# Kernel tuning notes

Measured on AMD Instinct MI355X. Metric: run time of the kernel, lower is better.

The kernel has to match this reference:

```python
import jax, jax.numpy as jnp
import numpy as np

N_NODES = 100000
N_EDGES = 1000000
D_IN = 64
D_OUT = 64


def setup_inputs() -> dict:
    key = jax.random.key(0)
    k1, k2, k3, k4, k5 = jax.random.split(key, 5)
    x = jax.random.normal(k1, (N_NODES, D_IN), dtype=jnp.float32)
    edge_val = jax.random.uniform(k2, (N_EDGES,), dtype=jnp.float32)
    # 'he' initializer: randn(in, out) * sqrt(2/in)
    weight = jax.random.normal(k3, (D_IN, D_OUT), dtype=jnp.float32) * np.sqrt(2.0 / D_IN)
    edge_src = jax.random.randint(k4, (N_EDGES,), 0, N_NODES, dtype=jnp.int32)
    edge_dst = jax.random.randint(k5, (N_EDGES,), 0, N_NODES, dtype=jnp.int32)
    return {"x": x, "edge_val": edge_val, "weight": weight,
            "edge_src": edge_src, "edge_dst": edge_dst}


def reference(x, edge_val, weight, edge_src, edge_dst):
    # order == 'AW': out = A @ x (SpMM over edge list) then @ W
    msgs = edge_val[:, None] * x[edge_src]                      # [E, D_IN]
    agg = jax.ops.segment_sum(msgs, edge_dst, num_segments=N_NODES)  # [N, D_IN]
    out = agg @ weight                                          # [N, D_OUT]
    # embnormalize: F.normalize(out, p=2, dim=1) with eps=1e-12
    norm = jnp.linalg.norm(out, axis=1, keepdims=True)
    out = out / jnp.maximum(norm, 1e-12)
    return jax.nn.relu(out)
```

## Files before the change

kernel.cpp:

```cpp
#include <hip/hip_runtime.h>
#include <hip/hip_bf16.h>

#define D 64

__global__ __launch_bounds__(256) void hist_kernel(
    const int* __restrict__ edge_dst, int* __restrict__ counts, int nEdges)
{
    int i = blockIdx.x * blockDim.x + threadIdx.x;
    int stride = gridDim.x * blockDim.x;
    for (; i < nEdges; i += stride)
        atomicAdd(&counts[edge_dst[i]], 1);
}

__global__ __launch_bounds__(256) void scanA_kernel(
    const int* __restrict__ counts, int* __restrict__ incl,
    int* __restrict__ blockSums, int n)
{
    __shared__ int buf[256];
    const int i = blockIdx.x * 256 + threadIdx.x;
    int v = (i < n) ? counts[i] : 0;
    buf[threadIdx.x] = v;
    __syncthreads();
    for (int off = 1; off < 256; off <<= 1) {
        int t = (threadIdx.x >= off) ? buf[threadIdx.x - off] : 0;
        __syncthreads();
        buf[threadIdx.x] += t;
        __syncthreads();
    }
    if (i < n) incl[i] = buf[threadIdx.x];
    if (threadIdx.x == 255) blockSums[blockIdx.x] = buf[255];
}

__global__ __launch_bounds__(1024) void scanB_kernel(int* __restrict__ bs, int nB)
{
    __shared__ int buf[1024];
    __shared__ int carry;
    if (threadIdx.x == 0) carry = 0;
    __syncthreads();
    for (int base = 0; base < nB; base += 1024) {
        const int i = base + (int)threadIdx.x;
        int v = (i < nB) ? bs[i] : 0;
        buf[threadIdx.x] = v;
        __syncthreads();
        for (int off = 1; off < 1024; off <<= 1) {
            int t = (threadIdx.x >= off) ? buf[threadIdx.x - off] : 0;
            __syncthreads();
            buf[threadIdx.x] += t;
            __syncthreads();
        }
        if (i < nB) bs[i] = buf[threadIdx.x] - v + carry;
        __syncthreads();
        if (threadIdx.x == 0) carry += buf[1023];
        __syncthreads();
    }
}

__global__ __launch_bounds__(256) void scanC_kernel(
    const int* __restrict__ counts, const int* __restrict__ incl,
    const int* __restrict__ blockSums, int* __restrict__ offsets,
    int* __restrict__ cursor, int n)
{
    const int i = blockIdx.x * 256 + threadIdx.x;
    if (i < n) {
        int off = incl[i] - counts[i] + blockSums[blockIdx.x];
        offsets[i] = off;
        cursor[i]  = off;
    }
}

__global__ __launch_bounds__(256) void scatter_kernel(
    const int*   __restrict__ edge_src,
    const int*   __restrict__ edge_dst,
    const float* __restrict__ edge_val,
    int*  __restrict__ cursor,
    int2* __restrict__ sorted_sv,
    int nEdges)
{
    int i = blockIdx.x * blockDim.x + threadIdx.x;
    int stride = gridDim.x * blockDim.x;
    for (; i < nEdges; i += stride) {
        const int d = edge_dst[i];
        const int pos = atomicAdd(&cursor[d], 1);
        sorted_sv[pos] = make_int2(edge_src[i], __float_as_int(edge_val[i]));
    }
}

__global__ __launch_bounds__(256) void gather_gemv_norm_kernel(
    const float* __restrict__ x,
    const float* __restrict__ W,
    const int*   __restrict__ offsets,
    const int*   __restrict__ counts,
    const int2*  __restrict__ sorted_sv,
    float*       __restrict__ out,
    int nNodes)
{
    __shared__ float Wlds[D * D];
    for (int i = threadIdx.x; i < D * D; i += blockDim.x)
        Wlds[i] = W[i];
    __syncthreads();

    const int lane   = threadIdx.x & 63;
    const int wave   = (blockIdx.x * blockDim.x + threadIdx.x) >> 6;
    const int nWaves = (gridDim.x * blockDim.x) >> 6;

    for (int n = wave; n < nNodes; n += nWaves) {
        const int start = offsets[n];
        const int cnt   = counts[n];

        float a0 = 0.f, a1 = 0.f, a2 = 0.f, a3 = 0.f;
        int j = start;
        const int end4 = start + (cnt & ~3);
        for (; j < end4; j += 4) {
            const int2 e0 = sorted_sv[j + 0];
            const int2 e1 = sorted_sv[j + 1];
            const int2 e2 = sorted_sv[j + 2];
            const int2 e3 = sorted_sv[j + 3];
            a0 += __int_as_float(e0.y) * x[(size_t)e0.x * D + lane];
            a1 += __int_as_float(e1.y) * x[(size_t)e1.x * D + lane];
            a2 += __int_as_float(e2.y) * x[(size_t)e2.x * D + lane];
            a3 += __int_as_float(e3.y) * x[(size_t)e3.x * D + lane];
        }
        const int end = start + cnt;
        for (; j < end; ++j) {
            const int2 e = sorted_sv[j];
            a0 += __int_as_float(e.y) * x[(size_t)e.x * D + lane];
        }
        const float acc = (a0 + a1) + (a2 + a3);

        float o = 0.f;
        #pragma unroll
        for (int k = 0; k < D; ++k)
            o += __shfl(acc, k, 64) * Wlds[k * D + lane];

        float ss = o * o;
        #pragma unroll
        for (int off = 32; off; off >>= 1)
            ss += __shfl_xor(ss, off, 64);
        const float inv = 1.f / fmaxf(sqrtf(ss), 1e-12f);

        out[(size_t)n * D + lane] = fmaxf(o * inv, 0.f);
    }
}

extern "C" void kernel_launch(void* const* d_in, const int* in_sizes, int n_in,
                              void* d_out, int out_size, void* d_ws, size_t ws_size,
                              hipStream_t stream)
{
    const float* x        = (const float*)d_in[0];
    const float* edge_val = (const float*)d_in[1];
    const float* weight   = (const float*)d_in[2];
    const int*   edge_src = (const int*)d_in[3];
    const int*   edge_dst = (const int*)d_in[4];

    const int nNodes = in_sizes[0] / D;
    const int nEdges = in_sizes[1];
    const int nB     = (nNodes + 255) / 256;

    int*  counts    = (int*)d_ws;
    int*  offsets   = counts  + nNodes;
    int*  cursor    = offsets + nNodes;
    int*  incl      = cursor  + nNodes;
    int*  blockSums = incl    + nNodes;
    int2* sorted_sv = (int2*)(blockSums + 4096);
    float* out      = (float*)d_out;

    hipMemsetAsync(counts, 0, (size_t)nNodes * sizeof(int), stream);

    hist_kernel<<<2048, 256, 0, stream>>>(edge_dst, counts, nEdges);

    scanA_kernel<<<nB, 256, 0, stream>>>(counts, incl, blockSums, nNodes);
    scanB_kernel<<<1, 1024, 0, stream>>>(blockSums, nB);
    scanC_kernel<<<nB, 256, 0, stream>>>(counts, incl, blockSums, offsets, cursor, nNodes);

    scatter_kernel<<<2048, 256, 0, stream>>>(
        edge_src, edge_dst, edge_val, cursor, sorted_sv, nEdges);

    gather_gemv_norm_kernel<<<2048, 256, 0, stream>>>(
        x, weight, offsets, counts, sorted_sv, out, nNodes);
}
```

Baseline: 356.1 us.

## Gather fp16 copy of x, fuse conversion into histogram, drop scan pass

Converts x to half precision inside the histogram kernel and gathers the half rows in the aggregation kernel, halving gather traffic. The single-block scanB pass is removed: each scanC block sums the preceding block totals itself. The GEMV now reads a transposed, padded W and the accumulator from LDS with float4 loads instead of 64 shuffles, and the scatter grid is doubled. This adds fp16 rounding error on inputs and relies on wave-synchronous LDS access without a barrier.

```diff
diff --git a/kernel.cpp b/kernel.cpp
--- a/kernel.cpp
+++ b/kernel.cpp
@@ -1,15 +1,31 @@
 #include <hip/hip_runtime.h>
-#include <hip/hip_bf16.h>
+#include <hip/hip_fp16.h>
 
 #define D 64
 
-__global__ __launch_bounds__(256) void hist_kernel(
-    const int* __restrict__ edge_dst, int* __restrict__ counts, int nEdges)
+__global__ __launch_bounds__(256) void hist_convert_kernel(
+    const int*    __restrict__ edge_dst,
+    int*          __restrict__ counts,
+    int nEdges,
+    const float4* __restrict__ x4,
+    uint2*        __restrict__ xhq,
+    int nQuads)
 {
-    int i = blockIdx.x * blockDim.x + threadIdx.x;
-    int stride = gridDim.x * blockDim.x;
-    for (; i < nEdges; i += stride)
-        atomicAdd(&counts[edge_dst[i]], 1);
+    const int tid    = blockIdx.x * blockDim.x + threadIdx.x;
+    const int stride = gridDim.x * blockDim.x;
+
+    for (int e = tid; e < nEdges; e += stride)
+        atomicAdd(&counts[edge_dst[e]], 1);
+
+    for (int q = tid; q < nQuads; q += stride) {
+        const float4 v = x4[q];
+        const __half2 lo = __floats2half2_rn(v.x, v.y);
+        const __half2 hi = __floats2half2_rn(v.z, v.w);
+        uint2 u;
+        u.x = *reinterpret_cast<const unsigned*>(&lo);
+        u.y = *reinterpret_cast<const unsigned*>(&hi);
+        xhq[q] = u;
+    }
 }
 
 __global__ __launch_bounds__(256) void scanA_kernel(
@@ -31,38 +47,25 @@
     if (threadIdx.x == 255) blockSums[blockIdx.x] = buf[255];
 }
 
-__global__ __launch_bounds__(1024) void scanB_kernel(int* __restrict__ bs, int nB)
-{
-    __shared__ int buf[1024];
-    __shared__ int carry;
-    if (threadIdx.x == 0) carry = 0;
-    __syncthreads();
-    for (int base = 0; base < nB; base += 1024) {
-        const int i = base + (int)threadIdx.x;
-        int v = (i < nB) ? bs[i] : 0;
-        buf[threadIdx.x] = v;
-        __syncthreads();
-        for (int off = 1; off < 1024; off <<= 1) {
-            int t = (threadIdx.x >= off) ? buf[threadIdx.x - off] : 0;
-            __syncthreads();
-            buf[threadIdx.x] += t;
-            __syncthreads();
-        }
-        if (i < nB) bs[i] = buf[threadIdx.x] - v + carry;
-        __syncthreads();
-        if (threadIdx.x == 0) carry += buf[1023];
-        __syncthreads();
-    }
-}
-
 __global__ __launch_bounds__(256) void scanC_kernel(
     const int* __restrict__ counts, const int* __restrict__ incl,
     const int* __restrict__ blockSums, int* __restrict__ offsets,
     int* __restrict__ cursor, int n)
 {
-    const int i = blockIdx.x * 256 + threadIdx.x;
+    __shared__ int red[256];
+    const int b = blockIdx.x;
+    int p = 0;
+    for (int t = threadIdx.x; t < b; t += 256) p += blockSums[t];
+    red[threadIdx.x] = p;
+    __syncthreads();
+    for (int off = 128; off; off >>= 1) {
+        if ((int)threadIdx.x < off) red[threadIdx.x] += red[threadIdx.x + off];
+        __syncthreads();
+    }
+    const int prefix = red[0];
+    const int i = b * 256 + (int)threadIdx.x;
     if (i < n) {
-        int off = incl[i] - counts[i] + blockSums[blockIdx.x];
+        const int off = incl[i] - counts[i] + prefix;
         offsets[i] = off;
         cursor[i]  = off;
     }
@@ -77,7 +80,7 @@
     int nEdges)
 {
     int i = blockIdx.x * blockDim.x + threadIdx.x;
-    int stride = gridDim.x * blockDim.x;
+    const int stride = gridDim.x * blockDim.x;
     for (; i < nEdges; i += stride) {
         const int d = edge_dst[i];
         const int pos = atomicAdd(&cursor[d], 1);
@@ -86,20 +89,25 @@
 }
 
 __global__ __launch_bounds__(256) void gather_gemv_norm_kernel(
-    const float* __restrict__ x,
-    const float* __restrict__ W,
-    const int*   __restrict__ offsets,
-    const int*   __restrict__ counts,
-    const int2*  __restrict__ sorted_sv,
-    float*       __restrict__ out,
+    const __half* __restrict__ xh,
+    const float*  __restrict__ W,
+    const int*    __restrict__ offsets,
+    const int*    __restrict__ counts,
+    const int2*   __restrict__ sorted_sv,
+    float*        __restrict__ out,
     int nNodes)
 {
-    __shared__ float Wlds[D * D];
-    for (int i = threadIdx.x; i < D * D; i += blockDim.x)
-        Wlds[i] = W[i];
+    __shared__ float Wt[D][D + 4];
+    __shared__ float accL[4][D];
+
+    for (int i = threadIdx.x; i < D * D; i += blockDim.x) {
+        const int k = i >> 6, j = i & 63;
+        Wt[j][k] = W[i];
+    }
     __syncthreads();
 
     const int lane   = threadIdx.x & 63;
+    const int w      = threadIdx.x >> 6;
     const int wave   = (blockIdx.x * blockDim.x + threadIdx.x) >> 6;
     const int nWaves = (gridDim.x * blockDim.x) >> 6;
 
@@ -115,22 +123,27 @@
             const int2 e1 = sorted_sv[j + 1];
             const int2 e2 = sorted_sv[j + 2];
             const int2 e3 = sorted_sv[j + 3];
-            a0 += __int_as_float(e0.y) * x[(size_t)e0.x * D + lane];
-            a1 += __int_as_float(e1.y) * x[(size_t)e1.x * D + lane];
-            a2 += __int_as_float(e2.y) * x[(size_t)e2.x * D + lane];
-            a3 += __int_as_float(e3.y) * x[(size_t)e3.x * D + lane];
+            a0 += __int_as_float(e0.y) * __half2float(xh[(size_t)e0.x * D + lane]);
+            a1 += __int_as_float(e1.y) * __half2float(xh[(size_t)e1.x * D + lane]);
+            a2 += __int_as_float(e2.y) * __half2float(xh[(size_t)e2.x * D + lane]);
+            a3 += __int_as_float(e3.y) * __half2float(xh[(size_t)e3.x * D + lane]);
         }
         const int end = start + cnt;
         for (; j < end; ++j) {
             const int2 e = sorted_sv[j];
-            a0 += __int_as_float(e.y) * x[(size_t)e.x * D + lane];
+            a0 += __int_as_float(e.y) * __half2float(xh[(size_t)e.x * D + lane]);
         }
         const float acc = (a0 + a1) + (a2 + a3);
 
+        accL[w][lane] = acc;
+
         float o = 0.f;
         #pragma unroll
-        for (int k = 0; k < D; ++k)
-            o += __shfl(acc, k, 64) * Wlds[k * D + lane];
+        for (int k = 0; k < D; k += 4) {
+            const float4 wv = *reinterpret_cast<const float4*>(&Wt[lane][k]);
+            const float4 av = *reinterpret_cast<const float4*>(&accL[w][k]);
+            o += av.x * wv.x + av.y * wv.y + av.z * wv.z + av.w * wv.w;
+        }
 
         float ss = o * o;
         #pragma unroll
@@ -155,26 +168,28 @@
     const int nNodes = in_sizes[0] / D;
     const int nEdges = in_sizes[1];
     const int nB     = (nNodes + 255) / 256;
+    const int nQuads = nNodes * D / 4;
 
-    int*  counts    = (int*)d_ws;
-    int*  offsets   = counts  + nNodes;
-    int*  cursor    = offsets + nNodes;
-    int*  incl      = cursor  + nNodes;
-    int*  blockSums = incl    + nNodes;
-    int2* sorted_sv = (int2*)(blockSums + 4096);
-    float* out      = (float*)d_out;
+    int*    counts    = (int*)d_ws;
+    int*    offsets   = counts  + nNodes;
+    int*    cursor    = offsets + nNodes;
+    int*    incl      = cursor  + nNodes;
+    int*    blockSums = incl    + nNodes;
+    int2*   sorted_sv = (int2*)(blockSums + 4096);
+    __half* xh        = (__half*)(sorted_sv + nEdges);
+    float*  out       = (float*)d_out;
 
     hipMemsetAsync(counts, 0, (size_t)nNodes * sizeof(int), stream);
 
-    hist_kernel<<<2048, 256, 0, stream>>>(edge_dst, counts, nEdges);
+    hist_convert_kernel<<<2048, 256, 0, stream>>>(
+        edge_dst, counts, nEdges, (const float4*)x, (uint2*)xh, nQuads);
 
     scanA_kernel<<<nB, 256, 0, stream>>>(counts, incl, blockSums, nNodes);
-    scanB_kernel<<<1, 1024, 0, stream>>>(blockSums, nB);
     scanC_kernel<<<nB, 256, 0, stream>>>(counts, incl, blockSums, offsets, cursor, nNodes);
 
-    scatter_kernel<<<2048, 256, 0, stream>>>(
+    scatter_kernel<<<4096, 256, 0, stream>>>(
         edge_src, edge_dst, edge_val, cursor, sorted_sv, nEdges);
 
     gather_gemv_norm_kernel<<<2048, 256, 0, stream>>>(
-        x, weight, offsets, counts, sorted_sv, out, nNodes);
+        xh, weight, offsets, counts, sorted_sv, out, nNodes);
 }
```

New measurement: 296.2 us. 1.2x faster.
